# Optimization experiments

Measured on AMD Instinct MI355X. Metric: run time of the kernel, lower is better.

Reference implementation:

```python
import jax, jax.numpy as jnp
import numpy as np

B, T, D = 1, 2048, 1024
H, HD, NH = 16, 64, 2        # heads, head_dim, num_householder
EPS = 1e-5                   # RMSNorm eps
SCALE = HD ** -0.5           # query scale (k_dim**-0.5)


def setup_inputs() -> dict:
    key = jax.random.key(0)
    ks = jax.random.split(key, 10)
    init = lambda k, shape: jax.random.normal(k, shape, jnp.float32) * (shape[0] ** -0.5)
    return {
        "x": jax.random.normal(ks[0], (B, T, D), jnp.float32),
        "Wq": init(ks[1], (D, H * HD)),
        "Wk": init(ks[2], (D, NH * H * HD)),
        "Wv": init(ks[3], (D, NH * H * HD)),
        "Wb": init(ks[4], (D, NH * H)),
        "Wa": init(ks[5], (D, H)),
        "A_log": jnp.log(jax.random.uniform(ks[6], (H,), jnp.float32, 1e-2, 16.0)),
        "dt_bias": jnp.zeros((H,), jnp.float32),
        "Wg": init(ks[7], (D, H * HD)),
        "norm_weight": jnp.ones((HD,), jnp.float32),
        "Wo": init(ks[8], (H * HD, D)),
    }


def _l2norm(t):
    return t * jax.lax.rsqrt(jnp.sum(t * t, -1, keepdims=True) + 1e-6)


def _forward(x, Wq, Wk, Wv, Wb, Wa, A_log, dt_bias, Wg, norm_weight, Wo):
    # projections; householder sub-steps interleaved along time -> length T*NH
    q = _l2norm((x @ Wq).reshape(B, T, H, HD)) * SCALE            # [B,T,H,HD]
    k = _l2norm((x @ Wk).reshape(B, T, NH, H, HD)).reshape(B, T * NH, H, HD)
    v = (x @ Wv).reshape(B, T * NH, H, HD)
    # allow_neg_eigval=True -> beta in (0,2)
    beta = 2.0 * jax.nn.sigmoid((x @ Wb).reshape(B, T * NH, H))
    # gated decay applied once per token (first sub-step), zeros for the rest
    g = -jnp.exp(A_log) * jax.nn.softplus(x @ Wa + dt_bias)       # [B,T,H]
    g = jnp.concatenate(
        [g[:, :, None], jnp.zeros((B, T, NH - 1, H), g.dtype)], axis=2
    ).reshape(B, T * NH, H)
    qf = jnp.repeat(q, NH, axis=1)  # only sub-step NH-1 outputs are kept

    def step(S, inp):
        # S: [B,H,HD_k,HD_v] recurrent state
        k_t, v_t, b_t, g_t, q_t = inp
        S = S * jnp.exp(g_t)[..., None, None]
        pred = jnp.einsum('bhk,bhkv->bhv', k_t, S)
        dv = (v_t - pred) * b_t[..., None]
        S = S + k_t[..., None] * dv[..., None, :]
        o = jnp.einsum('bhk,bhkv->bhv', q_t, S)
        return S, o

    tm = lambda a: jnp.swapaxes(a, 0, 1)  # time-major for scan
    S0 = jnp.zeros((B, H, HD, HD), x.dtype)
    _, o = jax.lax.scan(step, S0, (tm(k), tm(v), tm(beta), tm(g), tm(qf)))
    o = tm(o[NH - 1::NH])  # last householder sub-step per token -> [B,T,H,HD]

    # gated RMSNorm (FusedRMSNormGated with swish gate)
    o = o * jax.lax.rsqrt(jnp.mean(o * o, -1, keepdims=True) + EPS) * norm_weight
    gate = (x @ Wg).reshape(B, T, H, HD)
    o = o * (gate * jax.nn.sigmoid(gate))
    return o.reshape(B, T, H * HD) @ Wo


def reference(x, Wq, Wk, Wv, Wb, Wa, A_log, dt_bias, Wg, norm_weight, Wo):
    return _forward(x, Wq, Wk, Wv, Wb, Wa, A_log, dt_bias, Wg, norm_weight, Wo)
```

## Files before the change

### kernel.cpp

```cpp
#include <hip/hip_runtime.h>
#include <stdint.h>


typedef unsigned short u16;
typedef __attribute__((ext_vector_type(8))) short bf16x8;
typedef __attribute__((ext_vector_type(4))) float f32x4;
typedef __attribute__((ext_vector_type(2))) float f32x2;
typedef __attribute__((ext_vector_type(4))) unsigned short u16x4;

#define TT 2048
#define NP 6208
#define NC 64
#define CS 64

__device__ __forceinline__ u16 f2bf(float f) {
  union { float f; uint32_t u; } v; v.f = f;
  uint32_t r = v.u + 0x7fffu + ((v.u >> 16) & 1u);
  return (u16)(r >> 16);
}
__device__ __forceinline__ float bf2f(u16 b) {
  union { uint32_t u; float f; } v; v.u = ((uint32_t)b) << 16; return v.f;
}

__global__ void cvt_kernel(const float* __restrict__ src, u16* __restrict__ dst, long n) {
  long i = (long)blockIdx.x * 256 + threadIdx.x;
  if (i < n) dst[i] = f2bf(src[i]);
}

__global__ __launch_bounds__(256) void transAll_kernel(
    const float* __restrict__ Wq, const float* __restrict__ Wk,
    const float* __restrict__ Wv, const float* __restrict__ Wb,
    const float* __restrict__ Wa, const float* __restrict__ Wg,
    const float* __restrict__ Wo, u16* __restrict__ WT, u16* __restrict__ WoT) {
  int bx = blockIdx.x;
  const float* src; u16* dst; int cols;
  if      (bx < 32)  { src = Wq; dst = WT;                cols = 1024; }
  else if (bx < 96)  { src = Wk; dst = WT + 1024UL*1024;  cols = 2048; bx -= 32; }
  else if (bx < 160) { src = Wv; dst = WT + 3072UL*1024;  cols = 2048; bx -= 96; }
  else if (bx < 161) { src = Wb; dst = WT + 5120UL*1024;  cols = 32;   bx -= 160; }
  else if (bx < 162) { src = Wa; dst = WT + 5152UL*1024;  cols = 16;   bx -= 161; }
  else if (bx < 194) { src = Wg; dst = WT + 5168UL*1024;  cols = 1024; bx -= 162; }
  else               { src = Wo; dst = WoT;               cols = 1024; bx -= 194; }
  __shared__ float tile[32][33];
  const int tx = threadIdx.x & 31, ty = threadIdx.x >> 5;
  const int c0 = bx * 32, r0 = blockIdx.y * 32;
  for (int rr = ty; rr < 32; rr += 8)
    if (c0 + tx < cols) tile[rr][tx] = src[(size_t)(r0 + rr) * cols + c0 + tx];
  __syncthreads();
  for (int rr = ty; rr < 32; rr += 8)
    if (c0 + rr < cols) dst[(size_t)(c0 + rr) * 1024 + r0 + tx] = f2bf(tile[tx][rr]);
}

__global__ __launch_bounds__(256) void beacon_kernel(float* __restrict__ out, int n) {
  int i = blockIdx.x * 256 + threadIdx.x;
  if (i < n) out[i] = 4000.0f;
}

__global__ __launch_bounds__(256) void gemm128(const u16* __restrict__ A,
    const u16* __restrict__ BT, float* __restrict__ Cf, u16* __restrict__ Cb,
    int K, int lda, int ldc, int Nmax, int out_bf16) {
  const int bm = blockIdx.x * 128, bn = blockIdx.y * 128;
  const int tid = threadIdx.x, w = tid >> 6, lane = tid & 63;
  const int wr = (w >> 1) * 64, wc = (w & 1) * 64;
  const int quad = lane >> 4, r = lane & 15;
  __shared__ u16 As[128][40], Bs[128][40];
  f32x4 acc[4][4] = {};
  const int srow = tid >> 1, scg = (tid & 1) * 16;
  for (int ks = 0; ks < K; ks += 32) {
    bf16x8 a0 = *(const bf16x8*)(A  + (size_t)(bm + srow) * lda + ks + scg);
    bf16x8 a1 = *(const bf16x8*)(A  + (size_t)(bm + srow) * lda + ks + scg + 8);
    bf16x8 b0 = *(const bf16x8*)(BT + (size_t)(bn + srow) * K   + ks + scg);
    bf16x8 b1 = *(const bf16x8*)(BT + (size_t)(bn + srow) * K   + ks + scg + 8);
    __syncthreads();
    *(bf16x8*)&As[srow][scg]     = a0;
    *(bf16x8*)&As[srow][scg + 8] = a1;
    *(bf16x8*)&Bs[srow][scg]     = b0;
    *(bf16x8*)&Bs[srow][scg + 8] = b1;
    __syncthreads();
    bf16x8 af[4], bf[4];
#pragma unroll
    for (int i = 0; i < 4; i++) af[i] = *(const bf16x8*)&As[wr + i * 16 + r][quad * 8];
#pragma unroll
    for (int j = 0; j < 4; j++) bf[j] = *(const bf16x8*)&Bs[wc + j * 16 + r][quad * 8];
#pragma unroll
    for (int i = 0; i < 4; i++)
#pragma unroll
      for (int j = 0; j < 4; j++)
        acc[i][j] = __builtin_amdgcn_mfma_f32_16x16x32_bf16(af[i], bf[j], acc[i][j], 0, 0, 0);
  }
#pragma unroll
  for (int i = 0; i < 4; i++)
#pragma unroll
    for (int j = 0; j < 4; j++)
#pragma unroll
      for (int rg = 0; rg < 4; rg++) {
        int row = bm + wr + i * 16 + quad * 4 + rg;
        int col = bn + wc + j * 16 + r;
        if (col < Nmax) {
          float v = acc[i][j][rg];
          if (out_bf16) Cb[(size_t)row * ldc + col] = f2bf(v);
          else          Cf[(size_t)row * ldc + col] = v;
        }
      }
}

__global__ __launch_bounds__(64) void prep_kernel(float* __restrict__ P,
    const float* __restrict__ A_log, const float* __restrict__ dt_bias,
    float* __restrict__ betab, float* __restrict__ gbuf) {
  const int t = blockIdx.x >> 4, h = blockIdx.x & 15, lane = threadIdx.x;
  float* Pt = P + (size_t)t * NP;
  float qv = Pt[h * 64 + lane];
  float ss = qv * qv;
#pragma unroll
  for (int off = 32; off; off >>= 1) ss += __shfl_xor(ss, off);
  Pt[h * 64 + lane] = qv * rsqrtf(ss + 1e-6f) * 0.125f;
#pragma unroll
  for (int nh = 0; nh < 2; nh++) {
    float kv = Pt[1024 + nh * 1024 + h * 64 + lane];
    float ks = kv * kv;
#pragma unroll
    for (int off = 32; off; off >>= 1) ks += __shfl_xor(ks, off);
    Pt[1024 + nh * 1024 + h * 64 + lane] = kv * rsqrtf(ks + 1e-6f);
  }
  if (lane < 2) {
    float bb = Pt[5120 + lane * 16 + h];
    betab[(size_t)(2 * t + lane) * 16 + h] = 2.f / (1.f + expf(-bb));
  }
  if (lane == 0) {
    float a = Pt[5152 + h] + dt_bias[h];
    float sp = (a > 20.f) ? a : log1pf(expf(a));
    gbuf[t * 16 + h] = -expf(A_log[h]) * sp;
  }
}

__global__ __launch_bounds__(256, 1) void phaseA_kernel(const float* __restrict__ P,
    const float* __restrict__ betab, const float* __restrict__ gbuf,
    u16* __restrict__ Wbuf, u16* __restrict__ Uvbuf,
    float* __restrict__ Mbuf, float* __restrict__ NTbuf, float* __restrict__ cumbuf) {
  const int c = blockIdx.x, h = blockIdx.y, tid = threadIdx.x;
  const int bi = tid >> 4, bj = tid & 15;
  __shared__ float kf[64][68];
  __shared__ float kT[64][68];
  __shared__ float Tt[64][68];
  __shared__ float Sc[64][68];
  __shared__ float cumch[64], betach[64], bbch[64], rowfl[64];
  const size_t base = ((size_t)c * 16 + h) * 4096;

  for (int e = tid; e < 4096; e += 256) {
    int i = e >> 6, d = e & 63, s = c * 64 + i, t = s >> 1, nh = s & 1;
    float kv = P[(size_t)t * NP + 1024 + nh * 1024 + h * 64 + d];
    kf[i][d] = kv; kT[d][i] = kv;
  }
  if (tid < 64) betach[tid] = betab[(size_t)(c * 64 + tid) * 16 + h];
  __syncthreads();
  if (tid == 0) {
    float cum = 0.f;
    for (int i = 0; i < 64; i++) {
      if ((i & 1) == 0) cum += gbuf[(c * 32 + (i >> 1)) * 16 + h];
      cumch[i] = cum;
    }
  }
  __syncthreads();
  if (tid < 64) {
    bbch[tid] = betach[tid] * expf(cumch[tid]);
    rowfl[tid] = expf(cumch[63] - cumch[tid]);
  }
  {
    float acc[4][4] = {};
#pragma unroll 4
    for (int d = 0; d < 64; d++) {
      f32x4 a = *(const f32x4*)&kT[d][4 * bi];
      f32x4 b = *(const f32x4*)&kT[d][4 * bj];
#pragma unroll
      for (int rr = 0; rr < 4; rr++)
#pragma unroll
        for (int cc = 0; cc < 4; cc++) acc[rr][cc] += a[rr] * b[cc];
    }
#pragma unroll
    for (int rr = 0; rr < 4; rr++)
#pragma unroll
      for (int cc = 0; cc < 4; cc++) {
        int i = 4 * bi + rr, j = 4 * bj + cc;
        Sc[i][j] = (j < i) ? betach[i] * expf(cumch[i] - cumch[j]) * acc[rr][cc] : 0.f;
      }
  }
  __syncthreads();
  {
    int col = tid >> 2, part = tid & 3;
    if (part == 0) Tt[col][0] = (col == 0) ? 1.f : 0.f;
    for (int i = 1; i < 64; i++) {
      float partial = 0.f;
      for (int j = col + part; j < i; j += 4) partial += Sc[i][j] * Tt[col][j];
      partial += __shfl_xor(partial, 1);
      partial += __shfl_xor(partial, 2);
      if (part == 0) Tt[col][i] = ((i == col) ? 1.f : 0.f) - partial;
    }
  }
  __syncthreads();
  for (int e = tid; e < 4096; e += 256) {
    int i = e >> 6, d = e & 63, s = c * 64 + i, t = s >> 1, nh = s & 1;
    kT[i][d] = P[(size_t)t * NP + 3072 + nh * 1024 + h * 64 + d];
  }
  {
    float acc[4][4] = {};
#pragma unroll 4
    for (int j = 0; j < 4 * bi + 4; j++) {
      f32x4 tv = *(const f32x4*)&Tt[j][4 * bi];
      f32x4 kv = *(const f32x4*)&kf[j][4 * bj];
      float bbj = bbch[j];
#pragma unroll
      for (int rr = 0; rr < 4; rr++)
#pragma unroll
        for (int cc = 0; cc < 4; cc++) acc[rr][cc] += tv[rr] * bbj * kv[cc];
    }
#pragma unroll
    for (int rr = 0; rr < 4; rr++) {
      int i = 4 * bi + rr;
      u16x4 wb;
#pragma unroll
      for (int cc = 0; cc < 4; cc++) { Sc[i][4 * bj + cc] = acc[rr][cc]; wb[cc] = f2bf(acc[rr][cc]); }
      *(u16x4*)&Wbuf[base + (size_t)i * 64 + 4 * bj] = wb;
    }
  }
  __syncthreads();
  {
    const float bL = expf(cumch[63]);
    float acc[4][4] = {};
#pragma unroll 4
    for (int i = 0; i < 64; i++) {
      f32x4 kv = *(const f32x4*)&kf[i][4 * bi];
      f32x4 wv = *(const f32x4*)&Sc[i][4 * bj];
      float rf = rowfl[i];
#pragma unroll
      for (int rr = 0; rr < 4; rr++)
#pragma unroll
        for (int cc = 0; cc < 4; cc++) acc[rr][cc] += rf * kv[rr] * wv[cc];
    }
#pragma unroll
    for (int rr = 0; rr < 4; rr++) {
      int m = 4 * bi + rr;
      f32x4 mv;
#pragma unroll
      for (int cc = 0; cc < 4; cc++)
        mv[cc] = ((m == 4 * bj + cc) ? bL : 0.f) - acc[rr][cc];
      *(f32x4*)&Mbuf[base + (size_t)m * 64 + 4 * bj] = mv;
    }
  }
  __syncthreads();
  {
    float acc[4][4] = {};
#pragma unroll 4
    for (int j = 0; j < 4 * bi + 4; j++) {
      f32x4 tv = *(const f32x4*)&Tt[j][4 * bi];
      f32x4 vv = *(const f32x4*)&kT[j][4 * bj];
      float be = betach[j];
#pragma unroll
      for (int rr = 0; rr < 4; rr++)
#pragma unroll
        for (int cc = 0; cc < 4; cc++) acc[rr][cc] += tv[rr] * be * vv[cc];
    }
#pragma unroll
    for (int rr = 0; rr < 4; rr++) {
      int i = 4 * bi + rr;
      u16x4 ub;
#pragma unroll
      for (int cc = 0; cc < 4; cc++) { Sc[i][4 * bj + cc] = acc[rr][cc]; ub[cc] = f2bf(acc[rr][cc]); }
      *(u16x4*)&Uvbuf[base + (size_t)i * 64 + 4 * bj] = ub;
    }
  }
  __syncthreads();
  {
    float acc[4][4] = {};
#pragma unroll 4
    for (int i = 0; i < 64; i++) {
      f32x4 kv = *(const f32x4*)&kf[i][4 * bi];
      f32x4 uv = *(const f32x4*)&Sc[i][4 * bj];
      float rf = rowfl[i];
#pragma unroll
      for (int rr = 0; rr < 4; rr++)
#pragma unroll
        for (int cc = 0; cc < 4; cc++) acc[rr][cc] += rf * kv[rr] * uv[cc];
    }
#pragma unroll
    for (int cc = 0; cc < 4; cc++) {
      f32x4 nv;
#pragma unroll
      for (int rr = 0; rr < 4; rr++) nv[rr] = acc[rr][cc];
      *(f32x4*)&NTbuf[base + (size_t)(4 * bj + cc) * 64 + 4 * bi] = nv;
    }
  }
  if (tid < 64) cumbuf[((size_t)c * 16 + h) * 64 + tid] = cumch[tid];
}

__global__ __launch_bounds__(64) void phaseB_kernel(const float* __restrict__ Mbuf,
    const float* __restrict__ NTbuf, u16* __restrict__ S0Tbuf) {
  const int g = blockIdx.x, h = blockIdx.y, l = threadIdx.x;
  const int c0 = 2 * g, c1 = 2 * g + 1;
  __shared__ float Ssh[2][2][64];
  Ssh[0][0][l] = 0.f; Ssh[0][1][l] = 0.f;
  float s0 = 0.f, s1 = 0.f;
  f32x4 mreg[16];
  float n0, n1;
  {
    const float* Mc = Mbuf + (size_t)h * 4096 + (size_t)l * 64;
#pragma unroll
    for (int q = 0; q < 16; q++) mreg[q] = *(const f32x4*)(Mc + 4 * q);
    const float* Nc = NTbuf + (size_t)h * 4096;
    n0 = Nc[c0 * 64 + l]; n1 = Nc[c1 * 64 + l];
  }
  __syncthreads();
  int p = 0;
  for (int c = 0; c < NC; c++) {
    const size_t base = ((size_t)c * 16 + h) * 4096;
    S0Tbuf[base + (size_t)c0 * 64 + l] = f2bf(s0);
    S0Tbuf[base + (size_t)c1 * 64 + l] = f2bf(s1);
    f32x4 mnext[16]; float nn0 = 0.f, nn1 = 0.f;
    if (c + 1 < NC) {
      const float* Mn = Mbuf + ((size_t)(c + 1) * 16 + h) * 4096 + (size_t)l * 64;
#pragma unroll
      for (int q = 0; q < 16; q++) mnext[q] = *(const f32x4*)(Mn + 4 * q);
      const float* Nn = NTbuf + ((size_t)(c + 1) * 16 + h) * 4096;
      nn0 = Nn[c0 * 64 + l]; nn1 = Nn[c1 * 64 + l];
    }
    float acc0 = n0, acc1 = n1;
#pragma unroll
    for (int q = 0; q < 16; q++) {
      f32x4 mv = mreg[q];
      f32x4 sv0 = *(const f32x4*)&Ssh[p][0][4 * q];
      f32x4 sv1 = *(const f32x4*)&Ssh[p][1][4 * q];
#pragma unroll
      for (int t = 0; t < 4; t++) { acc0 += mv[t] * sv0[t]; acc1 += mv[t] * sv1[t]; }
    }
    s0 = acc0; s1 = acc1;
    Ssh[p ^ 1][0][l] = s0; Ssh[p ^ 1][1][l] = s1;
    __syncthreads();
    p ^= 1;
#pragma unroll
    for (int q = 0; q < 16; q++) mreg[q] = mnext[q];
    n0 = nn0; n1 = nn1;
  }
}

__global__ __launch_bounds__(256) void phaseB2_kernel(const u16* __restrict__ Wbuf,
    const u16* __restrict__ S0Tbuf, u16* __restrict__ Uvbuf) {
  const int c = blockIdx.x, h = blockIdx.y, tid = threadIdx.x;
  const int bi = tid >> 4, bd = tid & 15;
  __shared__ float WTl[64][68], S0l[64][68];
  const size_t base = ((size_t)c * 16 + h) * 4096;
  for (int e = tid; e < 4096; e += 256) {
    int i = e >> 6, m = e & 63;
    WTl[m][i] = bf2f(Wbuf[base + e]);
    S0l[m][i] = bf2f(S0Tbuf[base + e]);
  }
  __syncthreads();
  float acc[4][4] = {};
#pragma unroll 4
  for (int m = 0; m < 64; m++) {
    f32x4 wv = *(const f32x4*)&WTl[m][4 * bi];
    f32x4 sv = *(const f32x4*)&S0l[m][4 * bd];
#pragma unroll
    for (int rr = 0; rr < 4; rr++)
#pragma unroll
      for (int cc = 0; cc < 4; cc++) acc[rr][cc] += wv[rr] * sv[cc];
  }
#pragma unroll
  for (int rr = 0; rr < 4; rr++) {
    int i = 4 * bi + rr;
    u16x4 uv = *(const u16x4*)&Uvbuf[base + (size_t)i * 64 + 4 * bd];
    u16x4 ob;
#pragma unroll
    for (int cc = 0; cc < 4; cc++) ob[cc] = f2bf(bf2f(uv[cc]) - acc[rr][cc]);
    *(u16x4*)&Uvbuf[base + (size_t)i * 64 + 4 * bd] = ob;
  }
}

__global__ __launch_bounds__(256) void phaseC_kernel(const float* __restrict__ P,
    const float* __restrict__ cumbuf, const u16* __restrict__ Ubuf,
    const u16* __restrict__ S0Tbuf, const float* __restrict__ nw,
    u16* __restrict__ ybuf) {
  const int c = blockIdx.x, h = blockIdx.y, tid = threadIdx.x;
  const int rb = tid >> 4, jb = tid & 15;
  __shared__ float qT[64][36];
  __shared__ float kTc[64][68];
  __shared__ float Ul[64][68];
  __shared__ float PmT[64][36];
  __shared__ float cuml[64], nwl[64];
  const size_t base = (size_t)c * 16 + h;
  for (int e = tid; e < 2048; e += 256) {
    int r = e >> 6, d = e & 63;
    qT[d][r] = P[(size_t)(c * 32 + r) * NP + h * 64 + d];
  }
  for (int e = tid; e < 4096; e += 256) {
    int j = e >> 6, d = e & 63, s = c * 64 + j, t = s >> 1, nh = s & 1;
    kTc[d][j] = P[(size_t)t * NP + 1024 + nh * 1024 + h * 64 + d];
    Ul[j][d] = bf2f(Ubuf[base * 4096 + e]);
  }
  if (tid < 64) { cuml[tid] = cumbuf[base * 64 + tid]; nwl[tid] = nw[tid]; }
  __syncthreads();
  {
    float pa[2][4] = {};
#pragma unroll 4
    for (int d = 0; d < 64; d++) {
      f32x2 qv = *(const f32x2*)&qT[d][2 * rb];
      f32x4 kv = *(const f32x4*)&kTc[d][4 * jb];
#pragma unroll
      for (int rr = 0; rr < 2; rr++)
#pragma unroll
        for (int cc = 0; cc < 4; cc++) pa[rr][cc] += qv[rr] * kv[cc];
    }
#pragma unroll
    for (int rr = 0; rr < 2; rr++)
#pragma unroll
      for (int cc = 0; cc < 4; cc++) {
        int r = 2 * rb + rr, i = 2 * r + 1, j = 4 * jb + cc;
        PmT[j][r] = (j <= i) ? expf(cuml[i] - cuml[j]) * pa[rr][cc] : 0.f;
      }
  }
  __syncthreads();
  for (int e = tid; e < 4096; e += 256) {
    int d = e >> 6, m = e & 63;
    kTc[m][d] = bf2f(S0Tbuf[base * 4096 + e]);
  }
  __syncthreads();
  float o[2][4];
  {
    float a1[2][4] = {}, a2[2][4] = {};
#pragma unroll 4
    for (int m = 0; m < 64; m++) {
      f32x2 qv = *(const f32x2*)&qT[m][2 * rb];
      f32x4 sv = *(const f32x4*)&kTc[m][4 * jb];
#pragma unroll
      for (int rr = 0; rr < 2; rr++)
#pragma unroll
        for (int cc = 0; cc < 4; cc++) a1[rr][cc] += qv[rr] * sv[cc];
    }
#pragma unroll 4
    for (int j = 0; j < 4 * rb + 4; j++) {
      f32x2 pv = *(const f32x2*)&PmT[j][2 * rb];
      f32x4 uv = *(const f32x4*)&Ul[j][4 * jb];
#pragma unroll
      for (int rr = 0; rr < 2; rr++)
#pragma unroll
        for (int cc = 0; cc < 4; cc++) a2[rr][cc] += pv[rr] * uv[cc];
    }
#pragma unroll
    for (int rr = 0; rr < 2; rr++) {
      float ec = expf(cuml[2 * (2 * rb + rr) + 1]);
#pragma unroll
      for (int cc = 0; cc < 4; cc++) o[rr][cc] = a1[rr][cc] * ec + a2[rr][cc];
    }
  }
  __syncthreads();
  float* ol = &qT[0][0];
#pragma unroll
  for (int rr = 0; rr < 2; rr++)
#pragma unroll
    for (int cc = 0; cc < 4; cc++)
      ol[(2 * rb + rr) * 68 + 4 * jb + cc] = o[rr][cc];
  __syncthreads();
  for (int e = tid; e < 2048; e += 256) {
    int r = e >> 6, d = e & 63;
    float ov = ol[r * 68 + d];
    float ss = ov * ov;
#pragma unroll
    for (int off = 32; off; off >>= 1) ss += __shfl_xor(ss, off);
    float on = ov * rsqrtf(ss * (1.f / 64.f) + 1e-5f) * nwl[d];
    int t = c * 32 + r;
    float gt = P[(size_t)t * NP + 5168 + h * 64 + d];
    float sw = gt / (1.f + expf(-gt));
    ybuf[(size_t)t * 1024 + h * 64 + d] = f2bf(on * sw);
  }
}

extern "C" void kernel_launch(void* const* d_in, const int* in_sizes, int n_in,
                              void* d_out, int out_size, void* d_ws, size_t ws_size,
                              hipStream_t stream) {
  const float* x       = (const float*)d_in[0];
  const float* Wq      = (const float*)d_in[1];
  const float* Wk      = (const float*)d_in[2];
  const float* Wv      = (const float*)d_in[3];
  const float* Wb      = (const float*)d_in[4];
  const float* Wa      = (const float*)d_in[5];
  const float* A_log   = (const float*)d_in[6];
  const float* dt_bias = (const float*)d_in[7];
  const float* Wg      = (const float*)d_in[8];
  const float* nw      = (const float*)d_in[9];
  const float* Wo      = (const float*)d_in[10];
  float* out = (float*)d_out;

  char* w = (char*)d_ws;
  size_t used = 0;
  auto alloc = [&](size_t bytes) {
    char* p = w + used; used += (bytes + 255) & ~(size_t)255; return p;
  };
  u16*   xb    = (u16*)  alloc(2048UL * 1024 * 2);
  u16*   WT    = (u16*)  alloc(6272UL * 1024 * 2);
  u16*   WoT   = (u16*)  alloc(1024UL * 1024 * 2);
  float* P     = (float*)alloc(2048UL * NP * 4);
  float* betab = (float*)alloc(4096UL * 16 * 4);
  float* gbuf  = (float*)alloc(2048UL * 16 * 4);
  u16*   ybuf  = (u16*)  alloc(2048UL * 1024 * 2);
  u16*   Wbuf  = (u16*)  alloc((size_t)NC * 16 * 4096 * 2);
  u16*   Uvbuf = (u16*)  alloc((size_t)NC * 16 * 4096 * 2);
  u16*   S0Tb  = (u16*)  alloc((size_t)NC * 16 * 4096 * 2);
  float* Mbuf  = (float*)alloc((size_t)NC * 16 * 4096 * 4);
  float* NTbuf = (float*)alloc((size_t)NC * 16 * 4096 * 4);
  float* cumb  = (float*)alloc((size_t)NC * 16 * 64 * 4);

  auto tgrid = [](long n) { return dim3((unsigned)((n + 255) / 256)); };
  if (used > ws_size) {
    beacon_kernel<<<tgrid(out_size), 256, 0, stream>>>(out, out_size);
    return;
  }

  hipMemsetAsync(WT + 6192UL * 1024, 0, 80UL * 1024 * 2, stream);

  cvt_kernel<<<tgrid(2048L*1024), 256, 0, stream>>>(x, xb, 2048L * 1024);
  transAll_kernel<<<dim3(226, 32), 256, 0, stream>>>(Wq, Wk, Wv, Wb, Wa, Wg, Wo, WT, WoT);

  gemm128<<<dim3(16, 49), 256, 0, stream>>>(xb, WT, P, nullptr, 1024, 1024, NP, NP, 0);
  prep_kernel<<<dim3(2048 * 16), 64, 0, stream>>>(P, A_log, dt_bias, betab, gbuf);

  phaseA_kernel<<<dim3(NC, 16), 256, 0, stream>>>(P, betab, gbuf, Wbuf, Uvbuf, Mbuf, NTbuf, cumb);
  phaseB_kernel<<<dim3(32, 16), 64, 0, stream>>>(Mbuf, NTbuf, S0Tb);
  phaseB2_kernel<<<dim3(NC, 16), 256, 0, stream>>>(Wbuf, S0Tb, Uvbuf);
  phaseC_kernel<<<dim3(NC, 16), 256, 0, stream>>>(P, cumb, Uvbuf, S0Tb, nw, ybuf);

  gemm128<<<dim3(16, 8), 256, 0, stream>>>(ybuf, WoT, out, nullptr, 1024, 1024, 1024, 1024, 0);
}
```

Before: 446.9 us.

## Use direct global-to-LDS loads in GEMM and shrink phaseA shared memory

The GEMM tile loader now uses the global_load_lds builtin to copy bf16 data straight into unpadded shared tiles, with no staging through registers. The aim is to cut register pressure and instruction count in the load path, at the risk of LDS bank conflicts now that the row padding is gone. In phaseA, the four 64x68 shared buffers become three reused ones. The V rows are prefetched into registers earlier so their global latency overlaps compute, and the smaller LDS footprint may allow more resident blocks. This adds extra barriers and buffer-aliasing logic that must be ordered correctly.

```diff
diff --git a/kernel.cpp b/kernel.cpp
--- a/kernel.cpp
+++ b/kernel.cpp
@@ -20,6 +20,12 @@
 }
 __device__ __forceinline__ float bf2f(u16 b) {
   union { uint32_t u; float f; } v; v.u = ((uint32_t)b) << 16; return v.f;
+}
+
+__device__ __forceinline__ void gload_lds16(const u16* g, u16* l) {
+  __builtin_amdgcn_global_load_lds(
+      (__attribute__((address_space(1))) const void*)(uintptr_t)g,
+      (__attribute__((address_space(3))) void*)(uint32_t)(uintptr_t)l, 16, 0, 0);
 }
 
 __global__ void cvt_kernel(const float* __restrict__ src, u16* __restrict__ dst, long n) {
@@ -63,19 +69,24 @@
   const int tid = threadIdx.x, w = tid >> 6, lane = tid & 63;
   const int wr = (w >> 1) * 64, wc = (w & 1) * 64;
   const int quad = lane >> 4, r = lane & 15;
-  __shared__ u16 As[128][40], Bs[128][40];
+  __shared__ u16 As[128][32], Bs[128][32];
   f32x4 acc[4][4] = {};
-  const int srow = tid >> 1, scg = (tid & 1) * 16;
+  const int sr = w * 32 + (lane >> 2);
+  const int sc = (lane & 3) * 8;
+  const u16* gA0 = A  + (size_t)(bm + sr) * lda + sc;
+  const u16* gA1 = A  + (size_t)(bm + sr + 16) * lda + sc;
+  const u16* gB0 = BT + (size_t)(bn + sr) * K + sc;
+  const u16* gB1 = BT + (size_t)(bn + sr + 16) * K + sc;
+  u16* lA0 = &As[w * 32][0];
+  u16* lA1 = &As[w * 32 + 16][0];
+  u16* lB0 = &Bs[w * 32][0];
+  u16* lB1 = &Bs[w * 32 + 16][0];
   for (int ks = 0; ks < K; ks += 32) {
-    bf16x8 a0 = *(const bf16x8*)(A  + (size_t)(bm + srow) * lda + ks + scg);
-    bf16x8 a1 = *(const bf16x8*)(A  + (size_t)(bm + srow) * lda + ks + scg + 8);
-    bf16x8 b0 = *(const bf16x8*)(BT + (size_t)(bn + srow) * K   + ks + scg);
-    bf16x8 b1 = *(const bf16x8*)(BT + (size_t)(bn + srow) * K   + ks + scg + 8);
     __syncthreads();
-    *(bf16x8*)&As[srow][scg]     = a0;
-    *(bf16x8*)&As[srow][scg + 8] = a1;
-    *(bf16x8*)&Bs[srow][scg]     = b0;
-    *(bf16x8*)&Bs[srow][scg + 8] = b1;
+    gload_lds16(gA0 + ks, lA0);
+    gload_lds16(gA1 + ks, lA1);
+    gload_lds16(gB0 + ks, lB0);
+    gload_lds16(gB1 + ks, lB1);
     __syncthreads();
     bf16x8 af[4], bf[4];
 #pragma unroll
@@ -139,17 +150,16 @@
     float* __restrict__ Mbuf, float* __restrict__ NTbuf, float* __restrict__ cumbuf) {
   const int c = blockIdx.x, h = blockIdx.y, tid = threadIdx.x;
   const int bi = tid >> 4, bj = tid & 15;
-  __shared__ float kf[64][68];
-  __shared__ float kT[64][68];
-  __shared__ float Tt[64][68];
-  __shared__ float Sc[64][68];
+  __shared__ float LA[64][68];
+  __shared__ float LB[64][68];
+  __shared__ float LC[64][68];
   __shared__ float cumch[64], betach[64], bbch[64], rowfl[64];
   const size_t base = ((size_t)c * 16 + h) * 4096;
 
   for (int e = tid; e < 4096; e += 256) {
     int i = e >> 6, d = e & 63, s = c * 64 + i, t = s >> 1, nh = s & 1;
     float kv = P[(size_t)t * NP + 1024 + nh * 1024 + h * 64 + d];
-    kf[i][d] = kv; kT[d][i] = kv;
+    LB[i][d] = kv; LA[d][i] = kv;
   }
   if (tid < 64) betach[tid] = betab[(size_t)(c * 64 + tid) * 16 + h];
   __syncthreads();
@@ -169,8 +179,8 @@
     float acc[4][4] = {};
 #pragma unroll 4
     for (int d = 0; d < 64; d++) {
-      f32x4 a = *(const f32x4*)&kT[d][4 * bi];
-      f32x4 b = *(const f32x4*)&kT[d][4 * bj];
+      f32x4 a = *(const f32x4*)&LA[d][4 * bi];
+      f32x4 b = *(const f32x4*)&LA[d][4 * bj];
 #pragma unroll
       for (int rr = 0; rr < 4; rr++)
 #pragma unroll
@@ -181,32 +191,37 @@
 #pragma unroll
       for (int cc = 0; cc < 4; cc++) {
         int i = 4 * bi + rr, j = 4 * bj + cc;
-        Sc[i][j] = (j < i) ? betach[i] * expf(cumch[i] - cumch[j]) * acc[rr][cc] : 0.f;
+        LC[i][j] = (j < i) ? betach[i] * expf(cumch[i] - cumch[j]) * acc[rr][cc] : 0.f;
       }
   }
   __syncthreads();
   {
     int col = tid >> 2, part = tid & 3;
-    if (part == 0) Tt[col][0] = (col == 0) ? 1.f : 0.f;
+    if (part == 0) LA[col][0] = (col == 0) ? 1.f : 0.f;
     for (int i = 1; i < 64; i++) {
       float partial = 0.f;
-      for (int j = col + part; j < i; j += 4) partial += Sc[i][j] * Tt[col][j];
+      for (int j = col + part; j < i; j += 4) partial += LC[i][j] * LA[col][j];
       partial += __shfl_xor(partial, 1);
       partial += __shfl_xor(partial, 2);
-      if (part == 0) Tt[col][i] = ((i == col) ? 1.f : 0.f) - partial;
-    }
-  }
-  __syncthreads();
-  for (int e = tid; e < 4096; e += 256) {
-    int i = e >> 6, d = e & 63, s = c * 64 + i, t = s >> 1, nh = s & 1;
-    kT[i][d] = P[(size_t)t * NP + 3072 + nh * 1024 + h * 64 + d];
+      if (part == 0) LA[col][i] = ((i == col) ? 1.f : 0.f) - partial;
+    }
+  }
+  __syncthreads();
+  float vreg[16];
+  {
+    const int vi = tid >> 6, vd = tid & 63;
+#pragma unroll
+    for (int s = 0; s < 16; s++) {
+      int i = vi + 4 * s, ss = c * 64 + i, t = ss >> 1, nh = ss & 1;
+      vreg[s] = P[(size_t)t * NP + 3072 + nh * 1024 + h * 64 + vd];
+    }
   }
   {
     float acc[4][4] = {};
 #pragma unroll 4
     for (int j = 0; j < 4 * bi + 4; j++) {
-      f32x4 tv = *(const f32x4*)&Tt[j][4 * bi];
-      f32x4 kv = *(const f32x4*)&kf[j][4 * bj];
+      f32x4 tv = *(const f32x4*)&LA[j][4 * bi];
+      f32x4 kv = *(const f32x4*)&LB[j][4 * bj];
       float bbj = bbch[j];
 #pragma unroll
       for (int rr = 0; rr < 4; rr++)
@@ -218,7 +233,7 @@
       int i = 4 * bi + rr;
       u16x4 wb;
 #pragma unroll
-      for (int cc = 0; cc < 4; cc++) { Sc[i][4 * bj + cc] = acc[rr][cc]; wb[cc] = f2bf(acc[rr][cc]); }
+      for (int cc = 0; cc < 4; cc++) { LC[i][4 * bj + cc] = acc[rr][cc]; wb[cc] = f2bf(acc[rr][cc]); }
       *(u16x4*)&Wbuf[base + (size_t)i * 64 + 4 * bj] = wb;
     }
   }
@@ -228,8 +243,8 @@
     float acc[4][4] = {};
 #pragma unroll 4
     for (int i = 0; i < 64; i++) {
-      f32x4 kv = *(const f32x4*)&kf[i][4 * bi];
-      f32x4 wv = *(const f32x4*)&Sc[i][4 * bj];
+      f32x4 kv = *(const f32x4*)&LB[i][4 * bi];
+      f32x4 wv = *(const f32x4*)&LC[i][4 * bj];
       float rf = rowfl[i];
 #pragma unroll
       for (int rr = 0; rr < 4; rr++)
@@ -248,23 +263,32 @@
   }
   __syncthreads();
   {
-    float acc[4][4] = {};
+    const int vi = tid >> 6, vd = tid & 63;
+#pragma unroll
+    for (int s = 0; s < 16; s++) LC[vi + 4 * s][vd] = vreg[s];
+  }
+  __syncthreads();
+  float ua[4][4] = {};
+  {
 #pragma unroll 4
     for (int j = 0; j < 4 * bi + 4; j++) {
-      f32x4 tv = *(const f32x4*)&Tt[j][4 * bi];
-      f32x4 vv = *(const f32x4*)&kT[j][4 * bj];
+      f32x4 tv = *(const f32x4*)&LA[j][4 * bi];
+      f32x4 vv = *(const f32x4*)&LC[j][4 * bj];
       float be = betach[j];
 #pragma unroll
       for (int rr = 0; rr < 4; rr++)
 #pragma unroll
-        for (int cc = 0; cc < 4; cc++) acc[rr][cc] += tv[rr] * be * vv[cc];
-    }
+        for (int cc = 0; cc < 4; cc++) ua[rr][cc] += tv[rr] * be * vv[cc];
+    }
+  }
+  __syncthreads();
+  {
 #pragma unroll
     for (int rr = 0; rr < 4; rr++) {
       int i = 4 * bi + rr;
       u16x4 ub;
 #pragma unroll
-      for (int cc = 0; cc < 4; cc++) { Sc[i][4 * bj + cc] = acc[rr][cc]; ub[cc] = f2bf(acc[rr][cc]); }
+      for (int cc = 0; cc < 4; cc++) { LA[i][4 * bj + cc] = ua[rr][cc]; ub[cc] = f2bf(ua[rr][cc]); }
       *(u16x4*)&Uvbuf[base + (size_t)i * 64 + 4 * bj] = ub;
     }
   }
@@ -273,8 +297,8 @@
     float acc[4][4] = {};
 #pragma unroll 4
     for (int i = 0; i < 64; i++) {
-      f32x4 kv = *(const f32x4*)&kf[i][4 * bi];
-      f32x4 uv = *(const f32x4*)&Sc[i][4 * bj];
+      f32x4 kv = *(const f32x4*)&LB[i][4 * bi];
+      f32x4 uv = *(const f32x4*)&LA[i][4 * bj];
       float rf = rowfl[i];
 #pragma unroll
       for (int rr = 0; rr < 4; rr++)
```

Result: faster. 427.4 us (-4.4%).
